# Optimization experiments

Hardware: AMD Instinct MI355X
Metric: run time of the kernel (lower is better)

The kernel has to match this reference:

```python
import jax, jax.numpy as jnp
import numpy as np

N1, N2, D = 8192, 8192, 128

def setup_inputs() -> dict:
    key = jax.random.key(0)
    k1, k2, k3, k4 = jax.random.split(key, 4)
    X1 = jax.random.normal(k1, (N1, D), dtype=jnp.float32)
    X2 = jax.random.normal(k2, (N2, D), dtype=jnp.float32)
    task1 = jax.random.randint(k3, (N1,), 0, 2, dtype=jnp.int32)
    task2 = jax.random.randint(k4, (N2,), 0, 2, dtype=jnp.int32)
    # learned parameters (init values match module defaults: lengthscale=1, output_variance=1, b=0)
    log_l = jnp.zeros((D,), dtype=jnp.float32)          # log(1)
    log_theta_l = jnp.zeros((1,), dtype=jnp.float32)    # log(1)
    b = jnp.zeros((1,), dtype=jnp.float32)
    return {"X1": X1, "X2": X2, "log_l": log_l, "log_theta_l": log_theta_l,
            "b": b, "task1": task1, "task2": task2}

def reference(X1, X2, log_l, log_theta_l, b, task1, task2):
    l = jnp.exp(log_l)                      # (D,) ARD lengthscales
    A = X1 / l                              # (N1, D)
    B = X2 / l                              # (N2, D)
    # sum((a-b)^2) = |a|^2 + |b|^2 - 2 a.b  -> GEMM form, no (N1,N2,D) intermediate
    sq_dist = (jnp.sum(A * A, axis=1)[:, None]
               + jnp.sum(B * B, axis=1)[None, :]
               - 2.0 * (A @ B.T))
    sq_dist = jnp.maximum(sq_dist, 0.0)
    K_base = jnp.exp(log_theta_l[0]) * jnp.exp(-0.5 * sq_dist)   # (N1, N2)
    # lambda = clip(2/(1+exp(b)) - 1, 0, 1)
    lam = jnp.clip(2.0 / (1.0 + jnp.exp(b[0])) - 1.0, 0.0, 1.0)
    diff_task = task1[:, None] != task2[None, :]                 # (N1, N2) bool
    K = K_base * jnp.where(diff_task, lam, 1.0)
    return K
```

## Files before the change

### kernel.cpp

```cpp
#include <hip/hip_runtime.h>
#include <stdint.h>

typedef float f32x4 __attribute__((ext_vector_type(4)));
typedef int   i32x4 __attribute__((ext_vector_type(4)));
typedef __bf16 bf16x8 __attribute__((ext_vector_type(8)));

#define NN 8192
#define DDIM 128

#define APRIME_OFF 0u
#define BPRIME_OFF (8192u*512u)
#define NORM_OFF   (268435456u - 65536u)

__device__ __forceinline__ uint32_t pk2(__bf16 a, __bf16 b) {
    return (uint32_t)__builtin_bit_cast(unsigned short, a)
         | ((uint32_t)__builtin_bit_cast(unsigned short, b) << 16);
}

__device__ __forceinline__ void gload_lds16(const void* g, void* l) {
    __builtin_amdgcn_global_load_lds(
        (const __attribute__((address_space(1))) uint32_t*)g,
        (__attribute__((address_space(3))) uint32_t*)l,
        16, 0, 0);
}

__global__ __launch_bounds__(256) void prep_kernel(
    const float* __restrict__ X1, const float* __restrict__ X2,
    const float* __restrict__ log_l, char* __restrict__ outbuf)
{
    int t = threadIdx.x, wave = t >> 6, lane = t & 63;
    int row = blockIdx.x * 4 + wave;
    const float* X; uint32_t base; float* nrm;
    if (row < NN) {
        X = X1 + (size_t)row * DDIM;
        base = APRIME_OFF + (uint32_t)row * 512u;
        nrm = (float*)(outbuf + NORM_OFF) + row;
    } else {
        int r2 = row - NN;
        X = X2 + (size_t)r2 * DDIM;
        base = BPRIME_OFF + (uint32_t)r2 * 512u;
        nrm = (float*)(outbuf + NORM_OFF) + NN + r2;
    }
    int c0 = lane * 2;
    float2 x = *(const float2*)(X + c0);
    float a0 = x.x * __expf(-log_l[c0]);
    float a1 = x.y * __expf(-log_l[c0 + 1]);
    float ss = a0 * a0 + a1 * a1;
    #pragma unroll
    for (int o = 32; o; o >>= 1) ss += __shfl_down(ss, o);
    if (lane == 0) *nrm = ss;
    __bf16 h0 = (__bf16)a0, h1 = (__bf16)a1;
    __bf16 l0 = (__bf16)(a0 - (float)h0), l1 = (__bf16)(a1 - (float)h1);
    int m = lane >> 2;
    int c = m >> 2;
    int sh = m & 3;
    int sl = 4 | sh;
    int rs = row & 7;
    uint32_t offh = base + (uint32_t)c * 128u + (uint32_t)((sh ^ rs) * 16) + (uint32_t)(lane & 3) * 4u;
    uint32_t offl = base + (uint32_t)c * 128u + (uint32_t)((sl ^ rs) * 16) + (uint32_t)(lane & 3) * 4u;
    *(uint32_t*)(outbuf + offh) = pk2(h0, h1);
    *(uint32_t*)(outbuf + offl) = pk2(l0, l1);
}

__global__ __launch_bounds__(256, 3) void fast_kernel(
    const char* __restrict__ stash,
    const int* __restrict__ task1, const int* __restrict__ task2,
    const float* __restrict__ log_theta_l, const float* __restrict__ bparam,
    float* __restrict__ C)
{
    __shared__ __align__(16) char smem[32768];
    const int t = threadIdx.x;
    const int lane = t & 63, wv = t >> 6;
    const int lr = lane & 15, lg = lane >> 4;
    const float* n1g = (const float*)(stash + NORM_OFF);
    const float* n2g = n1g + NN;
    float logt = log_theta_l[0];
    float bb = bparam[0];
    float lam = fminf(fmaxf(2.f / (1.f + __expf(bb)) - 1.f, 0.f), 1.f);
    int wg = blockIdx.x;

    if (wg < 3840) {
        const int wr = wv >> 1, wc = wv & 1;
        int swz = (wg & 7) * 480 + (wg >> 3);
        int tm = 2 + (swz >> 6);
        int tn = swz & 63;
        const char* Abase = stash + APRIME_OFF + (size_t)tm * 128 * 512;
        const char* Bbase = stash + BPRIME_OFF + (size_t)tn * 128 * 512;

        f32x4 acc[4][4];
        #pragma unroll
        for (int i = 0; i < 4; ++i)
            #pragma unroll
            for (int j = 0; j < 4; ++j) acc[i][j] = (f32x4){0.f, 0.f, 0.f, 0.f};

        #define STAGE_F(c) do {                                                       \
            _Pragma("unroll")                                                         \
            for (int i = 0; i < 4; ++i) {                                             \
                int l = t + i * 256;                                                  \
                gload_lds16(Abase + (size_t)(l >> 3) * 512 + (c) * 128 + (l & 7) * 16,\
                            smem + l * 16);                                           \
                gload_lds16(Bbase + (size_t)(l >> 3) * 512 + (c) * 128 + (l & 7) * 16,\
                            smem + 16384 + l * 16);                                   \
            }                                                                         \
        } while (0)

        #define FRAGMM_F() do {                                                       \
            bf16x8 ah[4], bh[4], xf[4];                                               \
            _Pragma("unroll")                                                         \
            for (int mi = 0; mi < 4; ++mi) {                                          \
                int row = wr * 64 + mi * 16 + lr;                                     \
                ah[mi] = *(const bf16x8*)(smem + row * 128 + ((lg ^ (row & 7)) * 16));\
            }                                                                         \
            _Pragma("unroll")                                                         \
            for (int ni = 0; ni < 4; ++ni) {                                          \
                int row = wc * 64 + ni * 16 + lr;                                     \
                bh[ni] = *(const bf16x8*)(smem + 16384 + row * 128                    \
                          + ((lg ^ (row & 7)) * 16));                                 \
            }                                                                         \
            _Pragma("unroll")                                                         \
            for (int mi = 0; mi < 4; ++mi)                                            \
                _Pragma("unroll")                                                     \
                for (int ni = 0; ni < 4; ++ni)                                        \
                    acc[mi][ni] = __builtin_amdgcn_mfma_f32_16x16x32_bf16(            \
                        bh[ni], ah[mi], acc[mi][ni], 0, 0, 0);                        \
            _Pragma("unroll")                                                         \
            for (int mi = 0; mi < 4; ++mi) {                                          \
                int row = wr * 64 + mi * 16 + lr;                                     \
                xf[mi] = *(const bf16x8*)(smem + row * 128                            \
                          + (((4 | lg) ^ (row & 7)) * 16));                           \
            }                                                                         \
            _Pragma("unroll")                                                         \
            for (int mi = 0; mi < 4; ++mi)                                            \
                _Pragma("unroll")                                                     \
                for (int ni = 0; ni < 4; ++ni)                                        \
                    acc[mi][ni] = __builtin_amdgcn_mfma_f32_16x16x32_bf16(            \
                        bh[ni], xf[mi], acc[mi][ni], 0, 0, 0);                        \
            _Pragma("unroll")                                                         \
            for (int ni = 0; ni < 4; ++ni) {                                          \
                int row = wc * 64 + ni * 16 + lr;                                     \
                xf[ni] = *(const bf16x8*)(smem + 16384 + row * 128                    \
                          + (((4 | lg) ^ (row & 7)) * 16));                           \
            }                                                                         \
            _Pragma("unroll")                                                         \
            for (int mi = 0; mi < 4; ++mi)                                            \
                _Pragma("unroll")                                                     \
                for (int ni = 0; ni < 4; ++ni)                                        \
                    acc[mi][ni] = __builtin_amdgcn_mfma_f32_16x16x32_bf16(            \
                        xf[ni], ah[mi], acc[mi][ni], 0, 0, 0);                        \
        } while (0)

        STAGE_F(0);
        __syncthreads();
        FRAGMM_F();
        #pragma unroll
        for (int c = 1; c < 4; ++c) {
            __syncthreads();
            STAGE_F(c);
            __syncthreads();
            FRAGMM_F();
        }

        int rbase = tm * 128, cbase = tn * 128;
        #pragma unroll
        for (int mi = 0; mi < 4; ++mi) {
            int rowl = wr * 64 + mi * 16 + lr;
            float n1v = n1g[rbase + rowl];
            int t1v = task1[rbase + rowl];
            #pragma unroll
            for (int ni = 0; ni < 4; ++ni) {
                int coll = wc * 64 + ni * 16 + lg * 4;
                f32x4 n2v = *(const f32x4*)(n2g + cbase + coll);
                i32x4 t2v = *(const i32x4*)(task2 + cbase + coll);
                f32x4 kv;
                #pragma unroll
                for (int rix = 0; rix < 4; ++rix) {
                    float s = fmaxf(n1v + n2v[rix] - 2.f * acc[mi][ni][rix], 0.f);
                    float k = __expf(fmaf(-0.5f, s, logt));
                    kv[rix] = (t1v != t2v[rix]) ? k * lam : k;
                }
                *(f32x4*)(C + (size_t)(rbase + rowl) * NN + cbase + coll) = kv;
            }
        }
        #undef STAGE_F
        #undef FRAGMM_F
    } else {
        int wq = wg - 3840;
        int tn = wq >> 2;
        int q = wq & 3;
        int arow0 = 62 * 128 + (q >> 1) * 64;
        int brow0 = tn * 128 + (q & 1) * 64;
        const int wr = wv >> 1, wc = wv & 1;
        const char* Abase = stash + APRIME_OFF + (size_t)arow0 * 512;
        const char* Bbase = stash + BPRIME_OFF + (size_t)brow0 * 512;

        f32x4 acc[2][2];
        #pragma unroll
        for (int i = 0; i < 2; ++i)
            #pragma unroll
            for (int j = 0; j < 2; ++j) acc[i][j] = (f32x4){0.f, 0.f, 0.f, 0.f};

        #define STAGE_Q(c) do {                                                       \
            _Pragma("unroll")                                                         \
            for (int i = 0; i < 2; ++i) {                                             \
                int l = t + i * 256;                                                  \
                gload_lds16(Abase + (size_t)(l >> 3) * 512 + (c) * 128 + (l & 7) * 16,\
                            smem + l * 16);                                           \
                gload_lds16(Bbase + (size_t)(l >> 3) * 512 + (c) * 128 + (l & 7) * 16,\
                            smem + 8192 + l * 16);                                    \
            }                                                                         \
        } while (0)

        #define FRAGMM_Q() do {                                                       \
            bf16x8 ah[2], bh[2], xf[2];                                               \
            _Pragma("unroll")                                                         \
            for (int mi = 0; mi < 2; ++mi) {                                          \
                int row = wr * 32 + mi * 16 + lr;                                     \
                ah[mi] = *(const bf16x8*)(smem + row * 128 + ((lg ^ (row & 7)) * 16));\
            }                                                                         \
            _Pragma("unroll")                                                         \
            for (int ni = 0; ni < 2; ++ni) {                                          \
                int row = wc * 32 + ni * 16 + lr;                                     \
                bh[ni] = *(const bf16x8*)(smem + 8192 + row * 128                     \
                          + ((lg ^ (row & 7)) * 16));                                 \
            }                                                                         \
            _Pragma("unroll")                                                         \
            for (int mi = 0; mi < 2; ++mi)                                            \
                _Pragma("unroll")                                                     \
                for (int ni = 0; ni < 2; ++ni)                                        \
                    acc[mi][ni] = __builtin_amdgcn_mfma_f32_16x16x32_bf16(            \
                        bh[ni], ah[mi], acc[mi][ni], 0, 0, 0);                        \
            _Pragma("unroll")                                                         \
            for (int mi = 0; mi < 2; ++mi) {                                          \
                int row = wr * 32 + mi * 16 + lr;                                     \
                xf[mi] = *(const bf16x8*)(smem + row * 128                            \
                          + (((4 | lg) ^ (row & 7)) * 16));                           \
            }                                                                         \
            _Pragma("unroll")                                                         \
            for (int mi = 0; mi < 2; ++mi)                                            \
                _Pragma("unroll")                                                     \
                for (int ni = 0; ni < 2; ++ni)                                        \
                    acc[mi][ni] = __builtin_amdgcn_mfma_f32_16x16x32_bf16(            \
                        bh[ni], xf[mi], acc[mi][ni], 0, 0, 0);                        \
            _Pragma("unroll")                                                         \
            for (int ni = 0; ni < 2; ++ni) {                                          \
                int row = wc * 32 + ni * 16 + lr;                                     \
                xf[ni] = *(const bf16x8*)(smem + 8192 + row * 128                     \
                          + (((4 | lg) ^ (row & 7)) * 16));                           \
            }                                                                         \
            _Pragma("unroll")                                                         \
            for (int mi = 0; mi < 2; ++mi)                                            \
                _Pragma("unroll")                                                     \
                for (int ni = 0; ni < 2; ++ni)                                        \
                    acc[mi][ni] = __builtin_amdgcn_mfma_f32_16x16x32_bf16(            \
                        xf[ni], ah[mi], acc[mi][ni], 0, 0, 0);                        \
        } while (0)

        STAGE_Q(0);
        __syncthreads();
        FRAGMM_Q();
        #pragma unroll
        for (int c = 1; c < 4; ++c) {
            __syncthreads();
            STAGE_Q(c);
            __syncthreads();
            FRAGMM_Q();
        }

        #pragma unroll
        for (int mi = 0; mi < 2; ++mi) {
            int rowl = wr * 32 + mi * 16 + lr;
            float n1v = n1g[arow0 + rowl];
            int t1v = task1[arow0 + rowl];
            #pragma unroll
            for (int ni = 0; ni < 2; ++ni) {
                int coll = wc * 32 + ni * 16 + lg * 4;
                f32x4 n2v = *(const f32x4*)(n2g + brow0 + coll);
                i32x4 t2v = *(const i32x4*)(task2 + brow0 + coll);
                f32x4 kv;
                #pragma unroll
                for (int rix = 0; rix < 4; ++rix) {
                    float s = fmaxf(n1v + n2v[rix] - 2.f * acc[mi][ni][rix], 0.f);
                    float k = __expf(fmaf(-0.5f, s, logt));
                    kv[rix] = (t1v != t2v[rix]) ? k * lam : k;
                }
                *(f32x4*)(C + (size_t)(arow0 + rowl) * NN + brow0 + coll) = kv;
            }
        }
        #undef STAGE_Q
        #undef FRAGMM_Q
    }
}

#define RSTRIDE 80
#define SQ_AH 0
#define SQ_AL 5120
#define SQ_BH 10240
#define SQ_BL 15360
#define SQ_ILS 20480
#define SQ_N1  20992
#define SQ_N2  21504
#define SQ_TOT 22016

__device__ __forceinline__ void split4(f32x4 x, uint2& hi, uint2& lo) {
    __bf16 h0 = (__bf16)x[0], h1 = (__bf16)x[1], h2 = (__bf16)x[2], h3 = (__bf16)x[3];
    hi.x = pk2(h0, h1); hi.y = pk2(h2, h3);
    __bf16 l0 = (__bf16)(x[0] - (float)h0);
    __bf16 l1 = (__bf16)(x[1] - (float)h1);
    __bf16 l2 = (__bf16)(x[2] - (float)h2);
    __bf16 l3 = (__bf16)(x[3] - (float)h3);
    lo.x = pk2(l0, l1); lo.y = pk2(l2, l3);
}

__device__ __forceinline__ void lds_barrier() {
    asm volatile("s_waitcnt lgkmcnt(0)" ::: "memory");
    __builtin_amdgcn_sched_barrier(0);
    __builtin_amdgcn_s_barrier();
    __builtin_amdgcn_sched_barrier(0);
}

__global__ __launch_bounds__(256, 3) void slow_kernel(
    const float* __restrict__ X1, const float* __restrict__ X2,
    const float* __restrict__ log_l,
    const float* __restrict__ log_theta_l, const float* __restrict__ bparam,
    const int* __restrict__ task1, const int* __restrict__ task2,
    float* __restrict__ C)
{
    __shared__ __align__(16) char smem[SQ_TOT];
    float* const ils = (float*)(smem + SQ_ILS);
    float* const n1s = (float*)(smem + SQ_N1);
    float* const n2s = (float*)(smem + SQ_N2);

    const int t = threadIdx.x;
    const int lane = t & 63;
    const int wv = t >> 6;
    const int wr = wv >> 1, wc = wv & 1;
    const int lr = lane & 15, lg = lane >> 4;
    const int kq = t & 7;
    const int rg = t >> 3;

    int wg = blockIdx.x;
    int ti = wg >> 2;
    int tsel = ti >> 6;
    int tm = (tsel == 2) ? 63 : tsel;
    int tn = ti & 63;
    int q = wg & 3;
    int row0 = tm * 128 + (q >> 1) * 64;
    int col0 = tn * 128 + (q & 1) * 64;

    const float* Ag = X1 + (size_t)row0 * DDIM;
    const float* Bg = X2 + (size_t)col0 * DDIM;

    if (t < 128) ils[t] = __expf(-log_l[t]);

    f32x4 aV[2], bV[2];
    #pragma unroll
    for (int e = 0; e < 2; ++e) {
        aV[e] = *(const f32x4*)(Ag + (size_t)(e * 32 + rg) * DDIM + kq * 4);
        bV[e] = *(const f32x4*)(Bg + (size_t)(e * 32 + rg) * DDIM + kq * 4);
    }
    __syncthreads();

    float nA[2] = {0.f, 0.f};
    float nB[2] = {0.f, 0.f};
    f32x4 acc[2][2];
    #pragma unroll
    for (int i = 0; i < 2; ++i)
        #pragma unroll
        for (int j = 0; j < 2; ++j) acc[i][j] = (f32x4){0.f, 0.f, 0.f, 0.f};

    for (int c = 0; c < 4; ++c) {
        {
            f32x4 il4 = *(const f32x4*)(ils + c * 32 + kq * 4);
            #pragma unroll
            for (int e = 0; e < 2; ++e) {
                int rr = e * 32 + rg;
                f32x4 xa = aV[e] * il4;
                f32x4 xb = bV[e] * il4;
                nA[e] += xa[0]*xa[0] + xa[1]*xa[1] + xa[2]*xa[2] + xa[3]*xa[3];
                nB[e] += xb[0]*xb[0] + xb[1]*xb[1] + xb[2]*xb[2] + xb[3]*xb[3];
                uint2 hA, lA, hB, lB;
                split4(xa, hA, lA);
                split4(xb, hB, lB);
                int boff = rr * RSTRIDE + kq * 8;
                *(uint2*)(smem + SQ_AH + boff) = hA;
                *(uint2*)(smem + SQ_AL + boff) = lA;
                *(uint2*)(smem + SQ_BH + boff) = hB;
                *(uint2*)(smem + SQ_BL + boff) = lB;
            }
        }
        if (c < 3) {
            #pragma unroll
            for (int e = 0; e < 2; ++e) {
                aV[e] = *(const f32x4*)(Ag + (size_t)(e * 32 + rg) * DDIM + (c + 1) * 32 + kq * 4);
                bV[e] = *(const f32x4*)(Bg + (size_t)(e * 32 + rg) * DDIM + (c + 1) * 32 + kq * 4);
            }
        }
        lds_barrier();
        {
            bf16x8 ah[2], bh[2], xf[2];
            #pragma unroll
            for (int mi = 0; mi < 2; ++mi) {
                int off = (wr * 32 + mi * 16 + lr) * RSTRIDE + lg * 16;
                ah[mi] = *(const bf16x8*)(smem + SQ_AH + off);
            }
            #pragma unroll
            for (int ni = 0; ni < 2; ++ni) {
                int off = (wc * 32 + ni * 16 + lr) * RSTRIDE + lg * 16;
                bh[ni] = *(const bf16x8*)(smem + SQ_BH + off);
            }
            #pragma unroll
            for (int mi = 0; mi < 2; ++mi)
                #pragma unroll
                for (int ni = 0; ni < 2; ++ni)
                    acc[mi][ni] = __builtin_amdgcn_mfma_f32_16x16x32_bf16(bh[ni], ah[mi], acc[mi][ni], 0, 0, 0);
            #pragma unroll
            for (int mi = 0; mi < 2; ++mi) {
                int off = (wr * 32 + mi * 16 + lr) * RSTRIDE + lg * 16;
                xf[mi] = *(const bf16x8*)(smem + SQ_AL + off);
            }
            #pragma unroll
            for (int mi = 0; mi < 2; ++mi)
                #pragma unroll
                for (int ni = 0; ni < 2; ++ni)
                    acc[mi][ni] = __builtin_amdgcn_mfma_f32_16x16x32_bf16(bh[ni], xf[mi], acc[mi][ni], 0, 0, 0);
            #pragma unroll
            for (int ni = 0; ni < 2; ++ni) {
                int off = (wc * 32 + ni * 16 + lr) * RSTRIDE + lg * 16;
                xf[ni] = *(const bf16x8*)(smem + SQ_BL + off);
            }
            #pragma unroll
            for (int mi = 0; mi < 2; ++mi)
                #pragma unroll
                for (int ni = 0; ni < 2; ++ni)
                    acc[mi][ni] = __builtin_amdgcn_mfma_f32_16x16x32_bf16(xf[ni], ah[mi], acc[mi][ni], 0, 0, 0);
        }
        lds_barrier();
    }

    #pragma unroll
    for (int e = 0; e < 2; ++e) {
        #pragma unroll
        for (int off = 1; off < 8; off <<= 1) {
            nA[e] += __shfl_xor(nA[e], off);
            nB[e] += __shfl_xor(nB[e], off);
        }
    }
    if (kq == 0) {
        #pragma unroll
        for (int e = 0; e < 2; ++e) {
            n1s[e * 32 + rg] = nA[e];
            n2s[e * 32 + rg] = nB[e];
        }
    }
    __syncthreads();

    float logt = log_theta_l[0];
    float bb = bparam[0];
    float lam = fminf(fmaxf(2.f / (1.f + __expf(bb)) - 1.f, 0.f), 1.f);

    #pragma unroll
    for (int mi = 0; mi < 2; ++mi) {
        int rowl = wr * 32 + mi * 16 + lr;
        float n1v = n1s[rowl];
        int t1v = task1[row0 + rowl];
        #pragma unroll
        for (int ni = 0; ni < 2; ++ni) {
            int coll = wc * 32 + ni * 16 + lg * 4;
            f32x4 n2v = *(const f32x4*)(n2s + coll);
            i32x4 t2v = *(const i32x4*)(task2 + col0 + coll);
            f32x4 kv;
            #pragma unroll
            for (int rix = 0; rix < 4; ++rix) {
                float s = fmaxf(n1v + n2v[rix] - 2.f * acc[mi][ni][rix], 0.f);
                float k = __expf(fmaf(-0.5f, s, logt));
                kv[rix] = (t1v != t2v[rix]) ? k * lam : k;
            }
            *(f32x4*)(C + (size_t)(row0 + rowl) * NN + col0 + coll) = kv;
        }
    }
}

extern "C" void kernel_launch(void* const* d_in, const int* in_sizes, int n_in,
                              void* d_out, int out_size, void* d_ws, size_t ws_size,
                              hipStream_t stream)
{
    const float* X1 = (const float*)d_in[0];
    const float* X2 = (const float*)d_in[1];
    const float* log_l = (const float*)d_in[2];
    const float* log_theta = (const float*)d_in[3];
    const float* bp = (const float*)d_in[4];
    const int* t1 = (const int*)d_in[5];
    const int* t2 = (const int*)d_in[6];
    float* C = (float*)d_out;
    (void)d_ws; (void)ws_size; (void)in_sizes; (void)n_in; (void)out_size;

    prep_kernel<<<4096, 256, 0, stream>>>(X1, X2, log_l, (char*)d_out);
    fast_kernel<<<4096, 256, 0, stream>>>((const char*)d_out, t1, t2, log_theta, bp, C);
    slow_kernel<<<768, 256, 0, stream>>>(X1, X2, log_l, log_theta, bp, t1, t2, C);
}
```

Baseline: 97.95 us.

## Load MFMA fragments directly from global memory instead of staging through LDS

Measured after the change: 122.3 us. +24.9%, slower.

```diff
diff --git a/kernel.cpp b/kernel.cpp
--- a/kernel.cpp
+++ b/kernel.cpp
@@ -15,13 +15,6 @@
 __device__ __forceinline__ uint32_t pk2(__bf16 a, __bf16 b) {
     return (uint32_t)__builtin_bit_cast(unsigned short, a)
          | ((uint32_t)__builtin_bit_cast(unsigned short, b) << 16);
-}
-
-__device__ __forceinline__ void gload_lds16(const void* g, void* l) {
-    __builtin_amdgcn_global_load_lds(
-        (const __attribute__((address_space(1))) uint32_t*)g,
-        (__attribute__((address_space(3))) uint32_t*)l,
-        16, 0, 0);
 }
 
 __global__ __launch_bounds__(256) void prep_kernel(
@@ -68,7 +61,6 @@
     const float* __restrict__ log_theta_l, const float* __restrict__ bparam,
     float* __restrict__ C)
 {
-    __shared__ __align__(16) char smem[32768];
     const int t = threadIdx.x;
     const int lane = t & 63, wv = t >> 6;
     const int lr = lane & 15, lg = lane >> 4;
@@ -79,13 +71,17 @@
     float lam = fminf(fmaxf(2.f / (1.f + __expf(bb)) - 1.f, 0.f), 1.f);
     int wg = blockIdx.x;
 
+    const int uh = (lg ^ (lr & 7)) * 16;
+    const int ul = ((4 | lg) ^ (lr & 7)) * 16;
+
     if (wg < 3840) {
         const int wr = wv >> 1, wc = wv & 1;
         int swz = (wg & 7) * 480 + (wg >> 3);
         int tm = 2 + (swz >> 6);
         int tn = swz & 63;
-        const char* Abase = stash + APRIME_OFF + (size_t)tm * 128 * 512;
-        const char* Bbase = stash + BPRIME_OFF + (size_t)tn * 128 * 512;
+
+        const char* Arow = stash + APRIME_OFF + (size_t)(tm * 128 + wr * 64 + lr) * 512;
+        const char* Brow = stash + BPRIME_OFF + (size_t)(tn * 128 + wc * 64 + lr) * 512;
 
         f32x4 acc[4][4];
         #pragma unroll
@@ -93,71 +89,39 @@
             #pragma unroll
             for (int j = 0; j < 4; ++j) acc[i][j] = (f32x4){0.f, 0.f, 0.f, 0.f};
 
-        #define STAGE_F(c) do {                                                       \
-            _Pragma("unroll")                                                         \
-            for (int i = 0; i < 4; ++i) {                                             \
-                int l = t + i * 256;                                                  \
-                gload_lds16(Abase + (size_t)(l >> 3) * 512 + (c) * 128 + (l & 7) * 16,\
-                            smem + l * 16);                                           \
-                gload_lds16(Bbase + (size_t)(l >> 3) * 512 + (c) * 128 + (l & 7) * 16,\
-                            smem + 16384 + l * 16);                                   \
-            }                                                                         \
-        } while (0)
-
-        #define FRAGMM_F() do {                                                       \
-            bf16x8 ah[4], bh[4], xf[4];                                               \
-            _Pragma("unroll")                                                         \
-            for (int mi = 0; mi < 4; ++mi) {                                          \
-                int row = wr * 64 + mi * 16 + lr;                                     \
-                ah[mi] = *(const bf16x8*)(smem + row * 128 + ((lg ^ (row & 7)) * 16));\
-            }                                                                         \
-            _Pragma("unroll")                                                         \
-            for (int ni = 0; ni < 4; ++ni) {                                          \
-                int row = wc * 64 + ni * 16 + lr;                                     \
-                bh[ni] = *(const bf16x8*)(smem + 16384 + row * 128                    \
-                          + ((lg ^ (row & 7)) * 16));                                 \
-            }                                                                         \
-            _Pragma("unroll")                                                         \
-            for (int mi = 0; mi < 4; ++mi)                                            \
-                _Pragma("unroll")                                                     \
-                for (int ni = 0; ni < 4; ++ni)                                        \
-                    acc[mi][ni] = __builtin_amdgcn_mfma_f32_16x16x32_bf16(            \
-                        bh[ni], ah[mi], acc[mi][ni], 0, 0, 0);                        \
-            _Pragma("unroll")                                                         \
-            for (int mi = 0; mi < 4; ++mi) {                                          \
-                int row = wr * 64 + mi * 16 + lr;                                     \
-                xf[mi] = *(const bf16x8*)(smem + row * 128                            \
-                          + (((4 | lg) ^ (row & 7)) * 16));                           \
-            }                                                                         \
-            _Pragma("unroll")                                                         \
-            for (int mi = 0; mi < 4; ++mi)                                            \
-                _Pragma("unroll")                                                     \
-                for (int ni = 0; ni < 4; ++ni)                                        \
-                    acc[mi][ni] = __builtin_amdgcn_mfma_f32_16x16x32_bf16(            \
-                        bh[ni], xf[mi], acc[mi][ni], 0, 0, 0);                        \
-            _Pragma("unroll")                                                         \
-            for (int ni = 0; ni < 4; ++ni) {                                          \
-                int row = wc * 64 + ni * 16 + lr;                                     \
-                xf[ni] = *(const bf16x8*)(smem + 16384 + row * 128                    \
-                          + (((4 | lg) ^ (row & 7)) * 16));                           \
-            }                                                                         \
-            _Pragma("unroll")                                                         \
-            for (int mi = 0; mi < 4; ++mi)                                            \
-                _Pragma("unroll")                                                     \
-                for (int ni = 0; ni < 4; ++ni)                                        \
-                    acc[mi][ni] = __builtin_amdgcn_mfma_f32_16x16x32_bf16(            \
-                        xf[ni], ah[mi], acc[mi][ni], 0, 0, 0);                        \
-        } while (0)
-
-        STAGE_F(0);
-        __syncthreads();
-        FRAGMM_F();
-        #pragma unroll
-        for (int c = 1; c < 4; ++c) {
-            __syncthreads();
-            STAGE_F(c);
-            __syncthreads();
-            FRAGMM_F();
+        #pragma unroll
+        for (int c = 0; c < 4; ++c) {
+            bf16x8 ah[4], bh[4], xf[4];
+            #pragma unroll
+            for (int mi = 0; mi < 4; ++mi)
+                ah[mi] = *(const bf16x8*)(Arow + mi * 8192 + c * 128 + uh);
+            #pragma unroll
+            for (int ni = 0; ni < 4; ++ni)
+                bh[ni] = *(const bf16x8*)(Brow + ni * 8192 + c * 128 + uh);
+            #pragma unroll
+            for (int mi = 0; mi < 4; ++mi)
+                #pragma unroll
+                for (int ni = 0; ni < 4; ++ni)
+                    acc[mi][ni] = __builtin_amdgcn_mfma_f32_16x16x32_bf16(
+                        bh[ni], ah[mi], acc[mi][ni], 0, 0, 0);
+            #pragma unroll
+            for (int mi = 0; mi < 4; ++mi)
+                xf[mi] = *(const bf16x8*)(Arow + mi * 8192 + c * 128 + ul);
+            #pragma unroll
+            for (int mi = 0; mi < 4; ++mi)
+                #pragma unroll
+                for (int ni = 0; ni < 4; ++ni)
+                    acc[mi][ni] = __builtin_amdgcn_mfma_f32_16x16x32_bf16(
+                        bh[ni], xf[mi], acc[mi][ni], 0, 0, 0);
+            #pragma unroll
+            for (int ni = 0; ni < 4; ++ni)
+                xf[ni] = *(const bf16x8*)(Brow + ni * 8192 + c * 128 + ul);
+            #pragma unroll
+            for (int mi = 0; mi < 4; ++mi)
+                #pragma unroll
+                for (int ni = 0; ni < 4; ++ni)
+                    acc[mi][ni] = __builtin_amdgcn_mfma_f32_16x16x32_bf16(
+                        xf[ni], ah[mi], acc[mi][ni], 0, 0, 0);
         }
 
         int rbase = tm * 128, cbase = tn * 128;
@@ -181,8 +145,6 @@
                 *(f32x4*)(C + (size_t)(rbase + rowl) * NN + cbase + coll) = kv;
             }
         }
-        #undef STAGE_F
-        #undef FRAGMM_F
     } else {
         int wq = wg - 3840;
         int tn = wq >> 2;
@@ -190,8 +152,9 @@
         int arow0 = 62 * 128 + (q >> 1) * 64;
         int brow0 = tn * 128 + (q & 1) * 64;
         const int wr = wv >> 1, wc = wv & 1;
-        const char* Abase = stash + APRIME_OFF + (size_t)arow0 * 512;
-        const char* Bbase = stash + BPRIME_OFF + (size_t)brow0 * 512;
+
+        const char* Arow = stash + APRIME_OFF + (size_t)(arow0 + wr * 32 + lr) * 512;
+        const char* Brow = stash + BPRIME_OFF + (size_t)(brow0 + wc * 32 + lr) * 512;
 
         f32x4 acc[2][2];
         #pragma unroll
@@ -199,71 +162,39 @@
             #pragma unroll
             for (int j = 0; j < 2; ++j) acc[i][j] = (f32x4){0.f, 0.f, 0.f, 0.f};
 
-        #define STAGE_Q(c) do {                                                       \
-            _Pragma("unroll")                                                         \
-            for (int i = 0; i < 2; ++i) {                                             \
-                int l = t + i * 256;                                                  \
-                gload_lds16(Abase + (size_t)(l >> 3) * 512 + (c) * 128 + (l & 7) * 16,\
-                            smem + l * 16);                                           \
-                gload_lds16(Bbase + (size_t)(l >> 3) * 512 + (c) * 128 + (l & 7) * 16,\
-                            smem + 8192 + l * 16);                                    \
-            }                                                                         \
-        } while (0)
-
-        #define FRAGMM_Q() do {                                                       \
-            bf16x8 ah[2], bh[2], xf[2];                                               \
-            _Pragma("unroll")                                                         \
-            for (int mi = 0; mi < 2; ++mi) {                                          \
-                int row = wr * 32 + mi * 16 + lr;                                     \
-                ah[mi] = *(const bf16x8*)(smem + row * 128 + ((lg ^ (row & 7)) * 16));\
-            }                                                                         \
-            _Pragma("unroll")                                                         \
-            for (int ni = 0; ni < 2; ++ni) {                                          \
-                int row = wc * 32 + ni * 16 + lr;                                     \
-                bh[ni] = *(const bf16x8*)(smem + 8192 + row * 128                     \
-                          + ((lg ^ (row & 7)) * 16));                                 \
-            }                                                                         \
-            _Pragma("unroll")                                                         \
-            for (int mi = 0; mi < 2; ++mi)                                            \
-                _Pragma("unroll")                                                     \
-                for (int ni = 0; ni < 2; ++ni)                                        \
-                    acc[mi][ni] = __builtin_amdgcn_mfma_f32_16x16x32_bf16(            \
-                        bh[ni], ah[mi], acc[mi][ni], 0, 0, 0);                        \
-            _Pragma("unroll")                                                         \
-            for (int mi = 0; mi < 2; ++mi) {                                          \
-                int row = wr * 32 + mi * 16 + lr;                                     \
-                xf[mi] = *(const bf16x8*)(smem + row * 128                            \
-                          + (((4 | lg) ^ (row & 7)) * 16));                           \
-            }                                                                         \
-            _Pragma("unroll")                                                         \
-            for (int mi = 0; mi < 2; ++mi)                                            \
-                _Pragma("unroll")                                                     \
-                for (int ni = 0; ni < 2; ++ni)                                        \
-                    acc[mi][ni] = __builtin_amdgcn_mfma_f32_16x16x32_bf16(            \
-                        bh[ni], xf[mi], acc[mi][ni], 0, 0, 0);                        \
-            _Pragma("unroll")                                                         \
-            for (int ni = 0; ni < 2; ++ni) {                                          \
-                int row = wc * 32 + ni * 16 + lr;                                     \
-                xf[ni] = *(const bf16x8*)(smem + 8192 + row * 128                     \
-                          + (((4 | lg) ^ (row & 7)) * 16));                           \
-            }                                                                         \
-            _Pragma("unroll")                                                         \
-            for (int mi = 0; mi < 2; ++mi)                                            \
-                _Pragma("unroll")                                                     \
-                for (int ni = 0; ni < 2; ++ni)                                        \
-                    acc[mi][ni] = __builtin_amdgcn_mfma_f32_16x16x32_bf16(            \
-                        xf[ni], ah[mi], acc[mi][ni], 0, 0, 0);                        \
-        } while (0)
-
-        STAGE_Q(0);
-        __syncthreads();
-        FRAGMM_Q();
-        #pragma unroll
-        for (int c = 1; c < 4; ++c) {
-            __syncthreads();
-            STAGE_Q(c);
-            __syncthreads();
-            FRAGMM_Q();
+        #pragma unroll
+        for (int c = 0; c < 4; ++c) {
+            bf16x8 ah[2], bh[2], xf[2];
+            #pragma unroll
+            for (int mi = 0; mi < 2; ++mi)
+                ah[mi] = *(const bf16x8*)(Arow + mi * 8192 + c * 128 + uh);
+            #pragma unroll
+            for (int ni = 0; ni < 2; ++ni)
+                bh[ni] = *(const bf16x8*)(Brow + ni * 8192 + c * 128 + uh);
+            #pragma unroll
+            for (int mi = 0; mi < 2; ++mi)
+                #pragma unroll
+                for (int ni = 0; ni < 2; ++ni)
+                    acc[mi][ni] = __builtin_amdgcn_mfma_f32_16x16x32_bf16(
+                        bh[ni], ah[mi], acc[mi][ni], 0, 0, 0);
+            #pragma unroll
+            for (int mi = 0; mi < 2; ++mi)
+                xf[mi] = *(const bf16x8*)(Arow + mi * 8192 + c * 128 + ul);
+            #pragma unroll
+            for (int mi = 0; mi < 2; ++mi)
+                #pragma unroll
+                for (int ni = 0; ni < 2; ++ni)
+                    acc[mi][ni] = __builtin_amdgcn_mfma_f32_16x16x32_bf16(
+                        bh[ni], xf[mi], acc[mi][ni], 0, 0, 0);
+            #pragma unroll
+            for (int ni = 0; ni < 2; ++ni)
+                xf[ni] = *(const bf16x8*)(Brow + ni * 8192 + c * 128 + ul);
+            #pragma unroll
+            for (int mi = 0; mi < 2; ++mi)
+                #pragma unroll
+                for (int ni = 0; ni < 2; ++ni)
+                    acc[mi][ni] = __builtin_amdgcn_mfma_f32_16x16x32_bf16(
+                        xf[ni], ah[mi], acc[mi][ni], 0, 0, 0);
         }
 
         #pragma unroll
@@ -286,8 +217,6 @@
                 *(f32x4*)(C + (size_t)(arow0 + rowl) * NN + brow0 + coll) = kv;
             }
         }
-        #undef STAGE_Q
-        #undef FRAGMM_Q
     }
 }
 
```
